# Kernel tuning notes

Hardware: AMD Instinct MI355X
Metric: run time of the kernel (lower is better)

Reference implementation:

```python
import jax, jax.numpy as jnp
import numpy as np

B = 8
INPUT_SIZE = 32        # fc output dim == res row length
RESAMPLING = 500       # chunk width; 500->250->125->62->31 under 4 stride-2 pools
CHUNKS = 15            # == channel_size; seq length T = CHUNKS * RESAMPLING
T = CHUNKS * RESAMPLING
EPS = 1e-5
FC_IN = 32 * 6 * 31    # 5952 = flattened (C,H,W) embedding output


def _conv2d(x, w, b, pad):
    y = jax.lax.conv_general_dilated(x, w, (1, 1), pad,
                                     dimension_numbers=('NCHW', 'OIHW', 'NCHW'))
    return y + b[None, :, None, None]


def _bn(x, g, beta, m, v):
    # eval-mode BatchNorm2d with running stats
    scale = g / jnp.sqrt(v + EPS)
    return (x - m[None, :, None, None]) * scale[None, :, None, None] + beta[None, :, None, None]


def _maxpool22(x):
    return jax.lax.reduce_window(x, -jnp.inf, jax.lax.max, (1, 1, 2, 2), (1, 1, 2, 2), 'VALID')


def _forward(x, w1, b1, g1, beta1, m1, v1, w2, b2, g2, beta2, m2, v2,
             w3, b3, g3, beta3, m3, v3, w4, b4, g4, beta4, m4, v4,
             wfc, bfc, wc3, bc3, wout, bout):
    bsz = x.shape[0]
    # Vectorize the original per-sample / per-chunk Python loops:
    # split each [100, T] sample into CHUNKS windows of width RESAMPLING.
    h = x[:, 0].reshape(bsz, 100, CHUNKS, RESAMPLING)
    h = h.transpose(0, 2, 1, 3).reshape(bsz * CHUNKS, 1, 100, RESAMPLING)
    for w, b, g, bt, m, v in ((w1, b1, g1, beta1, m1, v1),
                              (w2, b2, g2, beta2, m2, v2),
                              (w3, b3, g3, beta3, m3, v3),
                              (w4, b4, g4, beta4, m4, v4)):
        h = _maxpool22(jax.nn.relu(_bn(_conv2d(h, w, b, [(2, 2), (2, 2)]), g, bt, m, v)))
    feats = h.reshape(bsz * CHUNKS, FC_IN)          # torch flattens in (C,H,W) order
    res = feats @ wfc.T + bfc                       # [B*15, 32]
    r = res.reshape(bsz, CHUNKS, INPUT_SIZE)[..., None]  # [B, 15, 32, 1] (NCHW)

    pad_c = lambda t: jnp.pad(t, ((0, 0), (0, 0), (1, 1), (0, 0)))   # ZeroPad2d((0,0,1,1))
    conv3 = lambda t: _conv2d(t, wc3, bc3, [(0, 0), (0, 0)])          # (3,1) conv
    r = conv3(jax.nn.relu(pad_c(r)))
    r = conv3(jax.nn.relu(pad_c(r)))
    while r.shape[2] > 2:  # static shapes: H 32->16->8->4->2
        p = jnp.pad(r, ((0, 0), (0, 0), (0, 1), (0, 0)))              # ZeroPad2d((0,0,0,1))
        px = jax.lax.reduce_window(p, -jnp.inf, jax.lax.max, (1, 1, 3, 1), (1, 1, 2, 2), 'VALID')
        t = conv3(jax.nn.relu(pad_c(px)))
        t = conv3(jax.nn.relu(pad_c(t)))
        r = t + px
    return r.reshape(bsz, 2 * CHUNKS) @ wout.T + bout  # [B, 2]


def setup_inputs() -> dict:
    key = jax.random.key(0)
    ks = jax.random.split(key, 16)

    def rn(k, shape, s):
        return jax.random.normal(k, shape, jnp.float32) * s

    inp = {"x": jax.random.normal(ks[0], (B, 1, 100, T), jnp.float32)}
    chans = [(1, 16), (16, 32), (32, 64), (64, 32)]
    for i, (ci, co) in enumerate(chans, 1):
        inp[f"w{i}"] = rn(ks[i], (co, ci, 5, 5), (2.0 / (ci * 25)) ** 0.5)
        inp[f"b{i}"] = jnp.zeros((co,), jnp.float32)
        inp[f"g{i}"] = jnp.ones((co,), jnp.float32)
        inp[f"beta{i}"] = jnp.zeros((co,), jnp.float32)
        inp[f"m{i}"] = jnp.zeros((co,), jnp.float32)
        inp[f"v{i}"] = jnp.ones((co,), jnp.float32)
    inp["wfc"] = rn(ks[5], (INPUT_SIZE, FC_IN), FC_IN ** -0.5)
    inp["bfc"] = jnp.zeros((INPUT_SIZE,), jnp.float32)
    inp["wc3"] = rn(ks[6], (CHUNKS, CHUNKS, 3, 1), (CHUNKS * 3) ** -0.5)
    inp["bc3"] = jnp.zeros((CHUNKS,), jnp.float32)
    inp["wout"] = rn(ks[7], (2, 2 * CHUNKS), (2 * CHUNKS) ** -0.5)
    inp["bout"] = jnp.zeros((2,), jnp.float32)
    return inp


def reference(x, w1, b1, g1, beta1, m1, v1, w2, b2, g2, beta2, m2, v2,
              w3, b3, g3, beta3, m3, v3, w4, b4, g4, beta4, m4, v4,
              wfc, bfc, wc3, bc3, wout, bout):
    return _forward(x, w1, b1, g1, beta1, m1, v1, w2, b2, g2, beta2, m2, v2,
                    w3, b3, g3, beta3, m3, v3, w4, b4, g4, beta4, m4, v4,
                    wfc, bfc, wc3, bc3, wout, bout)
```

## Files before the change

### kernel.cpp

```cpp
#include <hip/hip_runtime.h>
#include <hip/hip_bf16.h>

#define EPS 1e-5f

typedef short bf16x8 __attribute__((ext_vector_type(8)));
typedef float f32x4  __attribute__((ext_vector_type(4)));

__device__ __forceinline__ unsigned short f2bf(float f) {
    __hip_bfloat16 h = __float2bfloat16(f);
    return *(unsigned short*)&h;
}
__device__ __forceinline__ float bf2f(unsigned short u) {
    __hip_bfloat16 h = *(__hip_bfloat16*)&u;
    return __bfloat162float(h);
}

__device__ __forceinline__ void packA(const float* __restrict__ w,
                                      unsigned short* __restrict__ Apk,
                                      int i, int CI, int COTALL)
{
    const int j = i & 7, lane = (i >> 3) & 63, pc = i >> 9;
    const int p = pc / COTALL, cot = pc % COTALL;
    const int kidx = p * 32 + (lane >> 4) * 8 + j;
    const int tap = kidx / CI, ci = kidx % CI;
    const int co = cot * 16 + (lane & 15);
    Apk[i] = f2bf((tap < 25) ? w[((size_t)co * CI + ci) * 25 + tap] : 0.f);
}

__global__ void prep_all(
    const float* w1, const float* w2, const float* w3, const float* w4,
    const float* wfc,
    const float* g1, const float* be1, const float* m1, const float* v1, const float* b1,
    const float* g2, const float* be2, const float* m2, const float* v2, const float* b2,
    const float* g3, const float* be3, const float* m3, const float* v3, const float* b3,
    const float* g4, const float* be4, const float* m4, const float* v4, const float* b4,
    float* scsh, unsigned short* A1, unsigned short* A2, unsigned short* A3,
    unsigned short* A4, unsigned short* wfcT)
{
    constexpr int S0 = 144, S1 = S0 + 512, S2 = S1 + 13312;
    constexpr int S3 = S2 + 51200, S4 = S3 + 51200, S5 = S4 + 190464;
    const int idx = blockIdx.x * 256 + threadIdx.x;
    if (idx < S0) {
        const int t = idx;
        if (t < 32) {
            const float sc = g2[t] / sqrtf(v2[t] + EPS);
            scsh[t] = sc; scsh[32 + t] = (b2[t] - m2[t]) * sc + be2[t];
        } else if (t < 96) {
            const int c = t - 32;
            const float sc = g3[c] / sqrtf(v3[c] + EPS);
            scsh[64 + c] = sc; scsh[128 + c] = (b3[c] - m3[c]) * sc + be3[c];
        } else if (t < 128) {
            const int c = t - 96;
            const float sc = g4[c] / sqrtf(v4[c] + EPS);
            scsh[192 + c] = sc; scsh[224 + c] = (b4[c] - m4[c]) * sc + be4[c];
        } else {
            const int c = t - 128;
            const float sc = g1[c] / sqrtf(v1[c] + EPS);
            scsh[256 + c] = sc; scsh[272 + c] = (b1[c] - m1[c]) * sc + be1[c];
        }
    } else if (idx < S1) {
        const int i = idx - S0;
        const int j = i & 7, lane = i >> 3;
        const int k = ((lane >> 4) & 3) * 8 + j;
        A1[i] = f2bf((k < 25) ? w1[(lane & 15) * 25 + k] : 0.f);
    } else if (idx < S2) {
        packA(w2, A2, idx - S1, 16, 2);
    } else if (idx < S3) {
        packA(w3, A3, idx - S2, 32, 4);
    } else if (idx < S4) {
        packA(w4, A4, idx - S3, 64, 2);
    } else if (idx < S5) {
        const int i = idx - S4;
        const int o = i / 5952, j = i % 5952;
        const int c = j & 31, yx = j >> 5;
        wfcT[i] = f2bf(wfc[(size_t)o * 5952 + c * 186 + yx]);
    }
}

__global__ __launch_bounds__(256) void conv1_mfma(
    const float* __restrict__ x,
    const unsigned short* __restrict__ Apk1,
    const float* __restrict__ sc, const float* __restrict__ sh,
    unsigned short* __restrict__ out)
{
    constexpr int RSTR = 70;
    __shared__ unsigned short tile[12 * RSTR];
    const int n = blockIdx.z;
    const int y0 = blockIdx.y * 8, x0 = blockIdx.x * 64;
    const int b = n / 15, c = n % 15;
    const float* xb = x + (size_t)b * 100 * 7500 + (size_t)c * 500;
    const int tid = threadIdx.x;

    for (int i = tid; i < 12 * 68; i += 256) {
        const int yy = i / 68, xx = i % 68;
        const int gy = y0 - 2 + yy, gx = x0 - 2 + xx;
        float v = 0.f;
        if (gy >= 0 && gy < 100 && gx >= 0 && gx < 500) v = xb[gy * 7500 + gx];
        tile[yy * RSTR + xx] = f2bf(v);
    }

    const int lane = tid & 63, wav = tid >> 6;
    const int g = lane >> 4, c15 = lane & 15;
    const bf16x8 a = *(const bf16x8*)(Apk1 + lane * 8);

    int off[8];
    #pragma unroll
    for (int j = 0; j < 8; ++j) {
        int tap = g * 8 + j;
        if (tap > 24) tap = 24;
        off[j] = (tap / 5) * RSTR + (tap % 5);
    }
    __syncthreads();

    f32x4 acc[2][4] = {};
    #pragma unroll
    for (int r = 0; r < 2; ++r)
        #pragma unroll
        for (int cg = 0; cg < 4; ++cg) {
            const int base = (2 * wav + r) * RSTR + cg * 16 + c15;
            bf16x8 bfrag;
            #pragma unroll
            for (int j = 0; j < 8; ++j)
                ((unsigned short*)&bfrag)[j] = (short)tile[base + off[j]];
            acc[r][cg] = __builtin_amdgcn_mfma_f32_16x16x32_bf16(a, bfrag, acc[r][cg], 0, 0, 0);
        }

    const int py = blockIdx.y * 4 + wav;
    const float4 scv = *(const float4*)(sc + g * 4);
    const float4 shv = *(const float4*)(sh + g * 4);
    #pragma unroll
    for (int cg = 0; cg < 4; ++cg) {
        const int px = (x0 >> 1) + cg * 8 + (c15 >> 1);
        ushort4 st;
        #pragma unroll
        for (int reg = 0; reg < 4; ++reg) {
            const float scr = (&scv.x)[reg], shr = (&shv.x)[reg];
            const float v0 = fmaxf(acc[0][cg][reg] * scr + shr, 0.f);
            const float v1 = fmaxf(acc[1][cg][reg] * scr + shr, 0.f);
            float mx = fmaxf(v0, v1);
            mx = fmaxf(mx, __shfl_xor(mx, 1));
            (&st.x)[reg] = f2bf(mx);
        }
        if ((lane & 1) == 0 && py < 50 && px < 250)
            *(ushort4*)(out + (((size_t)n * 50 + py) * 250 + px) * 16 + g * 4) = st;
    }
}

template <int CI, int CO, int H, int W, int PH, int PW, int NP, int NCT>
__global__ __launch_bounds__(256) void mfma_conv(
    const unsigned short* __restrict__ in,
    const unsigned short* __restrict__ Apk,
    const float* __restrict__ sc, const float* __restrict__ sh,
    unsigned short* __restrict__ outp)
{
    constexpr int TH = 8, TW = 32, ROWS = TH + 4, COLS = TW + 4;
    constexpr int CPC = CI / 8;
    constexpr int PLANESZ = ROWS * COLS * 16;
    constexpr int PPAD = (CPC == 2) ? 64 : (CPC == 4 ? 32 : 16);
    constexpr int PSTR = PLANESZ + PPAD;
    constexpr int COTALL = CO / 16;
    constexpr int COB = CO / (16 * NCT);
    __shared__ char smem[CPC * PSTR];

    const int n = blockIdx.z / COB, cob = blockIdx.z % COB;
    const int ytile = blockIdx.y * TH, xtile = blockIdx.x * TW;
    const int tid = threadIdx.x;

    for (int i = tid; i < ROWS * COLS * CPC; i += 256) {
        const int cell = i / CPC, ch = i % CPC;
        const int yy = cell / COLS, xx = cell % COLS;
        const int gy = ytile - 2 + yy, gx = xtile - 2 + xx;
        uint4 val = make_uint4(0, 0, 0, 0);
        if (gy >= 0 && gy < H && gx >= 0 && gx < W)
            val = *(const uint4*)(in + ((((size_t)n * H + gy) * W + gx) * CI + ch * 8));
        *(uint4*)(smem + ch * PSTR + cell * 16) = val;
    }
    __syncthreads();

    const int lane = tid & 63, wav = tid >> 6;
    const int g = lane >> 4, c15 = lane & 15;
    const bool hi = (lane >= 32);
    const int plane = (CI == 16) ? (g & 1) : g;
    const char* bbase = smem + plane * PSTR + ((wav * 2) * COLS + c15) * 16;

    f32x4 acc[2][NCT][2] = {};

    #pragma unroll
    for (int p = 0; p < NP; ++p) {
        int Dv = 0;
        if (CI == 16) {
            int t0 = p * 2;     if (t0 > 24) t0 = 24;
            int t1 = p * 2 + 1; if (t1 > 24) t1 = 24;
            const int D0 = ((t0 / 5) * COLS + t0 % 5) * 16;
            const int D1 = ((t1 / 5) * COLS + t1 % 5) * 16;
            Dv = hi ? D1 : D0;
        }
        const int tap = (CI == 32) ? p : ((CI == 64) ? (p >> 1) : 0);
        const int pimm = (CI == 64) ? (p & 1) * 4 * PSTR : 0;

        bf16x8 a[NCT], b[2][2];
        #pragma unroll
        for (int ct = 0; ct < NCT; ++ct)
            a[ct] = *(const bf16x8*)(Apk +
                ((size_t)(p * COTALL + cob * NCT + ct) * 64 + lane) * 8);
        #pragma unroll
        for (int r = 0; r < 2; ++r)
            #pragma unroll
            for (int cg = 0; cg < 2; ++cg) {
                const int imm = (CI == 16)
                    ? (r * COLS + cg * 16) * 16
                    : (((r + tap / 5) * COLS + cg * 16 + tap % 5) * 16 + pimm);
                b[r][cg] = *(const bf16x8*)(bbase + Dv + imm);
            }
        #pragma unroll
        for (int r = 0; r < 2; ++r)
            #pragma unroll
            for (int ct = 0; ct < NCT; ++ct)
                #pragma unroll
                for (int cg = 0; cg < 2; ++cg)
                    acc[r][ct][cg] = __builtin_amdgcn_mfma_f32_16x16x32_bf16(
                        a[ct], b[r][cg], acc[r][ct][cg], 0, 0, 0);
    }

    const int py = blockIdx.y * 4 + wav;
    #pragma unroll
    for (int ct = 0; ct < NCT; ++ct) {
        const int coW = (cob * NCT + ct) * 16;
        const float4 scv = *(const float4*)(sc + coW + g * 4);
        const float4 shv = *(const float4*)(sh + coW + g * 4);
        #pragma unroll
        for (int cg = 0; cg < 2; ++cg) {
            const int px = (xtile >> 1) + cg * 8 + (c15 >> 1);
            ushort4 st;
            #pragma unroll
            for (int reg = 0; reg < 4; ++reg) {
                const float scr = (&scv.x)[reg], shr = (&shv.x)[reg];
                const float v0 = fmaxf(acc[0][ct][cg][reg] * scr + shr, 0.f);
                const float v1 = fmaxf(acc[1][ct][cg][reg] * scr + shr, 0.f);
                float mx = fmaxf(v0, v1);
                mx = fmaxf(mx, __shfl_xor(mx, 1));
                (&st.x)[reg] = f2bf(mx);
            }
            if ((lane & 1) == 0 && py < PH && px < PW)
                *(ushort4*)(outp + (((size_t)n * PH + py) * PW + px) * CO + coW + g * 4) = st;
        }
    }
}

__global__ __launch_bounds__(256) void fc_kernel(
    const unsigned short* __restrict__ feats, const unsigned short* __restrict__ wfcT,
    const float* __restrict__ bfc, float* __restrict__ res)
{
    const int n = blockIdx.x;
    const int lane = threadIdx.x & 63;
    const int wave = threadIdx.x >> 6;
    const unsigned short* f = feats + (size_t)n * 5952;
    #pragma unroll
    for (int o8 = 0; o8 < 8; ++o8) {
        const int o = wave * 8 + o8;
        const unsigned short* wr = wfcT + (size_t)o * 5952;
        float s = 0.f;
        #pragma unroll
        for (int i = 0; i < 12; ++i) {
            const int j8 = (i * 64 + lane) * 8;
            if (j8 < 5952) {
                const bf16x8 fv = *(const bf16x8*)(f + j8);
                const bf16x8 wv = *(const bf16x8*)(wr + j8);
                #pragma unroll
                for (int q = 0; q < 8; ++q)
                    s += bf2f(((const unsigned short*)&fv)[q]) *
                         bf2f(((const unsigned short*)&wv)[q]);
            }
        }
        #pragma unroll
        for (int off = 32; off > 0; off >>= 1) s += __shfl_down(s, off, 64);
        if (lane == 0) res[n * 32 + o] = s + bfc[o];
    }
}

__global__ __launch_bounds__(512) void dpcnn_kernel(
    const float* __restrict__ res,
    const float* __restrict__ wc3, const float* __restrict__ bc3,
    const float* __restrict__ wout, const float* __restrict__ bout,
    float* __restrict__ out)
{
    __shared__ float rr[8][15][32];
    __shared__ float ar[8][15][34];
    __shared__ float tr[8][15][34];
    __shared__ float px[8][15][16];
    __shared__ float wk[15][45];
    __shared__ float bk[15];

    const int tid = threadIdx.x;
    for (int i = tid; i < 15 * 45; i += 512) ((float*)wk)[i] = wc3[i];
    if (tid < 15) bk[tid] = bc3[tid];
    for (int i = tid; i < 8 * 15 * 32; i += 512) {
        const int h = i & 31, c = (i >> 5) % 15, b = i / 480;
        const float val = res[i];
        rr[b][c][h] = val;
        ar[b][c][h + 1] = fmaxf(val, 0.f);
    }
    for (int i = tid; i < 8 * 15; i += 512) {
        const int c = i % 15, b = i / 15;
        ar[b][c][0] = 0.f; ar[b][c][33] = 0.f;
        tr[b][c][0] = 0.f; tr[b][c][33] = 0.f;
    }
    __syncthreads();

    #define CONV45(SRC, BCH, CCH, HH)                                          \
        float s0 = bk[CCH], s1 = 0.f, s2 = 0.f;                                \
        {                                                                      \
            const float* srow = &SRC[BCH][0][HH];                              \
            const float* wrow = &wk[CCH][0];                                   \
            _Pragma("unroll")                                                  \
            for (int ci = 0; ci < 15; ++ci) {                                  \
                s0 += wrow[ci * 3 + 0] * srow[ci * 34 + 0];                    \
                s1 += wrow[ci * 3 + 1] * srow[ci * 34 + 1];                    \
                s2 += wrow[ci * 3 + 2] * srow[ci * 34 + 2];                    \
            }                                                                  \
        }                                                                      \
        const float val = s0 + s1 + s2;

    {
        for (int i = tid; i < 8 * 15 * 32; i += 512) {
            const int h = i & 31, cc = (i >> 5) % 15, b = i / 480;
            CONV45(ar, b, cc, h)
            tr[b][cc][h + 1] = fmaxf(val, 0.f);
        }
        __syncthreads();
        for (int i = tid; i < 8 * 15 * 32; i += 512) {
            const int h = i & 31, cc = (i >> 5) % 15, b = i / 480;
            CONV45(tr, b, cc, h)
            rr[b][cc][h] = val;
            ar[b][cc][h + 1] = fmaxf(val, 0.f);
        }
        __syncthreads();
    }

    for (int H = 32; H > 2; H >>= 1) {
        const int Hh = H >> 1;
        const int NE = 8 * 15 * Hh;
        for (int i = tid; i < NE; i += 512) {
            const int h = i % Hh, cc = (i / Hh) % 15, b = i / (15 * Hh);
            const float m0 = rr[b][cc][2 * h], m1 = rr[b][cc][2 * h + 1];
            const float m2 = (2 * h + 2 < H) ? rr[b][cc][2 * h + 2] : 0.f;
            const float pv = fmaxf(fmaxf(m0, m1), m2);
            px[b][cc][h] = pv;
            ar[b][cc][h + 1] = fmaxf(pv, 0.f);
            if (h == 0) ar[b][cc][0] = 0.f;
            if (h == Hh - 1) ar[b][cc][Hh + 1] = 0.f;
        }
        __syncthreads();
        for (int i = tid; i < NE; i += 512) {
            const int h = i % Hh, cc = (i / Hh) % 15, b = i / (15 * Hh);
            CONV45(ar, b, cc, h)
            tr[b][cc][h + 1] = fmaxf(val, 0.f);
            if (h == 0) tr[b][cc][0] = 0.f;
            if (h == Hh - 1) tr[b][cc][Hh + 1] = 0.f;
        }
        __syncthreads();
        for (int i = tid; i < NE; i += 512) {
            const int h = i % Hh, cc = (i / Hh) % 15, b = i / (15 * Hh);
            CONV45(tr, b, cc, h)
            const float rv = val + px[b][cc][h];
            rr[b][cc][h] = rv;
            ar[b][cc][h + 1] = fmaxf(rv, 0.f);
        }
        __syncthreads();
    }
    #undef CONV45

    if (tid < 16) {
        const int b = tid >> 1, o = tid & 1;
        float s = bout[o];
        for (int c = 0; c < 15; ++c)
            #pragma unroll
            for (int h = 0; h < 2; ++h)
                s += wout[o * 30 + c * 2 + h] * rr[b][c][h];
        out[b * 2 + o] = s;
    }
}

extern "C" void kernel_launch(void* const* d_in, const int* in_sizes, int n_in,
                              void* d_out, int out_size, void* d_ws, size_t ws_size,
                              hipStream_t stream)
{
    const float* x = (const float*)d_in[0];
    const float* w1 = (const float*)d_in[1];  const float* b1 = (const float*)d_in[2];
    const float* g1 = (const float*)d_in[3];  const float* be1 = (const float*)d_in[4];
    const float* m1 = (const float*)d_in[5];  const float* v1 = (const float*)d_in[6];
    const float* w2 = (const float*)d_in[7];  const float* b2 = (const float*)d_in[8];
    const float* g2 = (const float*)d_in[9];  const float* be2 = (const float*)d_in[10];
    const float* m2 = (const float*)d_in[11]; const float* v2 = (const float*)d_in[12];
    const float* w3 = (const float*)d_in[13]; const float* b3 = (const float*)d_in[14];
    const float* g3 = (const float*)d_in[15]; const float* be3 = (const float*)d_in[16];
    const float* m3 = (const float*)d_in[17]; const float* v3 = (const float*)d_in[18];
    const float* w4 = (const float*)d_in[19]; const float* b4 = (const float*)d_in[20];
    const float* g4 = (const float*)d_in[21]; const float* be4 = (const float*)d_in[22];
    const float* m4 = (const float*)d_in[23]; const float* v4 = (const float*)d_in[24];
    const float* wfc = (const float*)d_in[25]; const float* bfc = (const float*)d_in[26];
    const float* wc3 = (const float*)d_in[27]; const float* bc3 = (const float*)d_in[28];
    const float* wout = (const float*)d_in[29]; const float* bout = (const float*)d_in[30];
    float* out = (float*)d_out;

    (void)in_sizes; (void)n_in; (void)out_size; (void)ws_size;

    float* wsf = (float*)d_ws;
    float* res   = wsf;
    float* scsh  = wsf + 3840;
    float* sc2 = scsh, *sh2 = scsh + 32;
    float* sc3 = scsh + 64, *sh3 = scsh + 128;
    float* sc4 = scsh + 192, *sh4 = scsh + 224;
    float* sc1 = scsh + 256, *sh1 = scsh + 272;
    unsigned short* A1  = (unsigned short*)(wsf + 4160);
    unsigned short* A2  = (unsigned short*)(wsf + 4416);
    unsigned short* A3  = (unsigned short*)(wsf + 11072);
    unsigned short* A4  = (unsigned short*)(wsf + 36672);
    unsigned short* c1o = (unsigned short*)(wsf + 62272);
    unsigned short* c2o = (unsigned short*)(wsf + 12062272);
    unsigned short* c3o = (unsigned short*)(wsf + 18062272);
    unsigned short* c4o = (unsigned short*)(wsf + 20919232);
    unsigned short* wfcT = (unsigned short*)(wsf + 21276352);

    prep_all<<<1199, 256, 0, stream>>>(
        w1, w2, w3, w4, wfc,
        g1, be1, m1, v1, b1, g2, be2, m2, v2, b2,
        g3, be3, m3, v3, b3, g4, be4, m4, v4, b4,
        scsh, A1, A2, A3, A4, wfcT);

    conv1_mfma<<<dim3(8, 13, 120), 256, 0, stream>>>(x, A1, sc1, sh1, c1o);
    mfma_conv<16, 32, 50, 250, 25, 125, 13, 2><<<dim3(8, 7, 120), 256, 0, stream>>>(
        c1o, A2, sc2, sh2, c2o);
    mfma_conv<32, 64, 25, 125, 12, 62, 25, 4><<<dim3(4, 3, 120), 256, 0, stream>>>(
        c2o, A3, sc3, sh3, c3o);
    mfma_conv<64, 32, 12, 62, 6, 31, 50, 2><<<dim3(2, 2, 120), 256, 0, stream>>>(
        c3o, A4, sc4, sh4, c4o);
    fc_kernel<<<dim3(120), 256, 0, stream>>>(c4o, wfcT, bfc, res);
    dpcnn_kernel<<<dim3(1), 512, 0, stream>>>(res, wc3, bc3, wout, bout, out);
}
```

Measured before the change: 322.8 us.

## Fuse conv4 with FC layer per sample and widen conv2 tiles

Conv4 and the fully connected layer now run in one 512-thread kernel per sample. It stages the conv3 output in 16-channel slices through shared memory, keeps the pooled features in LDS and computes the FC dot products directly from them. This removes one launch and the global round trip of the conv4 output. The A4 weight packing is changed to match the new per-16-channel tap-pair order. The conv template gains a tile-width parameter and conv2 uses 64-wide tiles, halving its grid width. Only 120 blocks run the fused kernel, with 6 of 8 waves doing MFMA work, so parallelism may drop.

New measurement: 306.7 us. 5.0% less time.

```diff
diff --git a/kernel.cpp b/kernel.cpp
--- a/kernel.cpp
+++ b/kernel.cpp
@@ -38,7 +38,7 @@
     unsigned short* A4, unsigned short* wfcT)
 {
     constexpr int S0 = 144, S1 = S0 + 512, S2 = S1 + 13312;
-    constexpr int S3 = S2 + 51200, S4 = S3 + 51200, S5 = S4 + 190464;
+    constexpr int S3 = S2 + 51200, S4 = S3 + 53248, S5 = S4 + 190464;
     const int idx = blockIdx.x * 256 + threadIdx.x;
     if (idx < S0) {
         const int t = idx;
@@ -68,7 +68,15 @@
     } else if (idx < S3) {
         packA(w3, A3, idx - S2, 32, 4);
     } else if (idx < S4) {
-        packA(w4, A4, idx - S3, 64, 2);
+        const int i = idx - S3;
+        const int j = i & 7, lane = (i >> 3) & 63, pc = i >> 9;
+        const int p = pc >> 1, ct = pc & 1;
+        const int g = lane >> 4;
+        const int tp = p % 13, qt = p / 13;
+        const int tap = tp * 2 + (g >> 1);
+        const int ci = qt * 16 + (g & 1) * 8 + j;
+        const int co = ct * 16 + (lane & 15);
+        A4[i] = f2bf((tap < 25) ? w4[((size_t)co * 64 + ci) * 25 + tap] : 0.f);
     } else if (idx < S5) {
         const int i = idx - S4;
         const int o = i / 5952, j = i % 5952;
@@ -146,14 +154,14 @@
     }
 }
 
-template <int CI, int CO, int H, int W, int PH, int PW, int NP, int NCT>
+template <int CI, int CO, int H, int W, int PH, int PW, int NP, int NCT, int TWP>
 __global__ __launch_bounds__(256) void mfma_conv(
     const unsigned short* __restrict__ in,
     const unsigned short* __restrict__ Apk,
     const float* __restrict__ sc, const float* __restrict__ sh,
     unsigned short* __restrict__ outp)
 {
-    constexpr int TH = 8, TW = 32, ROWS = TH + 4, COLS = TW + 4;
+    constexpr int TH = 8, COLS = TWP + 4, ROWS = TH + 4, NCG = TWP / 16;
     constexpr int CPC = CI / 8;
     constexpr int PLANESZ = ROWS * COLS * 16;
     constexpr int PPAD = (CPC == 2) ? 64 : (CPC == 4 ? 32 : 16);
@@ -163,7 +171,7 @@
     __shared__ char smem[CPC * PSTR];
 
     const int n = blockIdx.z / COB, cob = blockIdx.z % COB;
-    const int ytile = blockIdx.y * TH, xtile = blockIdx.x * TW;
+    const int ytile = blockIdx.y * TH, xtile = blockIdx.x * TWP;
     const int tid = threadIdx.x;
 
     for (int i = tid; i < ROWS * COLS * CPC; i += 256) {
@@ -183,7 +191,7 @@
     const int plane = (CI == 16) ? (g & 1) : g;
     const char* bbase = smem + plane * PSTR + ((wav * 2) * COLS + c15) * 16;
 
-    f32x4 acc[2][NCT][2] = {};
+    f32x4 acc[2][NCT][NCG] = {};
 
     #pragma unroll
     for (int p = 0; p < NP; ++p) {
@@ -198,7 +206,7 @@
         const int tap = (CI == 32) ? p : ((CI == 64) ? (p >> 1) : 0);
         const int pimm = (CI == 64) ? (p & 1) * 4 * PSTR : 0;
 
-        bf16x8 a[NCT], b[2][2];
+        bf16x8 a[NCT], b[2][NCG];
         #pragma unroll
         for (int ct = 0; ct < NCT; ++ct)
             a[ct] = *(const bf16x8*)(Apk +
@@ -206,7 +214,7 @@
         #pragma unroll
         for (int r = 0; r < 2; ++r)
             #pragma unroll
-            for (int cg = 0; cg < 2; ++cg) {
+            for (int cg = 0; cg < NCG; ++cg) {
                 const int imm = (CI == 16)
                     ? (r * COLS + cg * 16) * 16
                     : (((r + tap / 5) * COLS + cg * 16 + tap % 5) * 16 + pimm);
@@ -217,7 +225,7 @@
             #pragma unroll
             for (int ct = 0; ct < NCT; ++ct)
                 #pragma unroll
-                for (int cg = 0; cg < 2; ++cg)
+                for (int cg = 0; cg < NCG; ++cg)
                     acc[r][ct][cg] = __builtin_amdgcn_mfma_f32_16x16x32_bf16(
                         a[ct], b[r][cg], acc[r][ct][cg], 0, 0, 0);
     }
@@ -229,7 +237,7 @@
         const float4 scv = *(const float4*)(sc + coW + g * 4);
         const float4 shv = *(const float4*)(sh + coW + g * 4);
         #pragma unroll
-        for (int cg = 0; cg < 2; ++cg) {
+        for (int cg = 0; cg < NCG; ++cg) {
             const int px = (xtile >> 1) + cg * 8 + (c15 >> 1);
             ushort4 st;
             #pragma unroll
@@ -247,24 +255,108 @@
     }
 }
 
-__global__ __launch_bounds__(256) void fc_kernel(
-    const unsigned short* __restrict__ feats, const unsigned short* __restrict__ wfcT,
+__global__ __launch_bounds__(512) void conv4fc_kernel(
+    const unsigned short* __restrict__ in,
+    const unsigned short* __restrict__ Apk,
+    const float* __restrict__ sc, const float* __restrict__ sh,
+    const unsigned short* __restrict__ wfcT,
     const float* __restrict__ bfc, float* __restrict__ res)
 {
+    constexpr int COLS = 66, ROWS = 16;
+    constexpr int PLANESZ = ROWS * COLS * 16;
+    constexpr int PSTR = PLANESZ + 32;
+    __shared__ char smem[2 * PSTR + 6 * 31 * 32 * 2];
+    unsigned short* feats = (unsigned short*)(smem + 2 * PSTR);
+
     const int n = blockIdx.x;
-    const int lane = threadIdx.x & 63;
-    const int wave = threadIdx.x >> 6;
-    const unsigned short* f = feats + (size_t)n * 5952;
+    const int tid = threadIdx.x;
+    const int lane = tid & 63, wav = tid >> 6;
+    const int g = lane >> 4, c15 = lane & 15;
+    const bool hi = (lane >= 32);
+
+    const char* bbase = smem + (g & 1) * PSTR + ((wav * 2) * COLS + c15) * 16;
+    f32x4 acc[2][2][4] = {};
+
+    for (int qt = 0; qt < 4; ++qt) {
+        __syncthreads();
+        for (int i = tid; i < ROWS * COLS * 2; i += 512) {
+            const int pl = i & 1, cell = i >> 1;
+            const int row = cell / COLS, col = cell - row * COLS;
+            const int gy = row - 2, gx = col - 2;
+            uint4 val = make_uint4(0, 0, 0, 0);
+            if (gy >= 0 && gy < 12 && gx >= 0 && gx < 62)
+                val = *(const uint4*)(in +
+                    ((((size_t)n * 12 + gy) * 62 + gx) * 64 + qt * 16 + pl * 8));
+            *(uint4*)(smem + pl * PSTR + cell * 16) = val;
+        }
+        __syncthreads();
+        if (wav < 6) {
+            #pragma unroll
+            for (int tp = 0; tp < 13; ++tp) {
+                const int p = qt * 13 + tp;
+                int t0 = tp * 2;     if (t0 > 24) t0 = 24;
+                int t1 = tp * 2 + 1; if (t1 > 24) t1 = 24;
+                const int D0 = ((t0 / 5) * COLS + t0 % 5) * 16;
+                const int D1 = ((t1 / 5) * COLS + t1 % 5) * 16;
+                const int Dv = hi ? D1 : D0;
+                bf16x8 a[2], b[2][4];
+                #pragma unroll
+                for (int ct = 0; ct < 2; ++ct)
+                    a[ct] = *(const bf16x8*)(Apk + ((size_t)(p * 2 + ct) * 64 + lane) * 8);
+                #pragma unroll
+                for (int r = 0; r < 2; ++r)
+                    #pragma unroll
+                    for (int cg = 0; cg < 4; ++cg)
+                        b[r][cg] = *(const bf16x8*)(bbase + Dv + (r * COLS + cg * 16) * 16);
+                #pragma unroll
+                for (int r = 0; r < 2; ++r)
+                    #pragma unroll
+                    for (int ct = 0; ct < 2; ++ct)
+                        #pragma unroll
+                        for (int cg = 0; cg < 4; ++cg)
+                            acc[r][ct][cg] = __builtin_amdgcn_mfma_f32_16x16x32_bf16(
+                                a[ct], b[r][cg], acc[r][ct][cg], 0, 0, 0);
+            }
+        }
+    }
+
+    if (wav < 6) {
+        const int py = wav;
+        #pragma unroll
+        for (int ct = 0; ct < 2; ++ct) {
+            const int coW = ct * 16;
+            const float4 scv = *(const float4*)(sc + coW + g * 4);
+            const float4 shv = *(const float4*)(sh + coW + g * 4);
+            #pragma unroll
+            for (int cg = 0; cg < 4; ++cg) {
+                const int px = cg * 8 + (c15 >> 1);
+                ushort4 st;
+                #pragma unroll
+                for (int reg = 0; reg < 4; ++reg) {
+                    const float scr = (&scv.x)[reg], shr = (&shv.x)[reg];
+                    const float v0 = fmaxf(acc[0][ct][cg][reg] * scr + shr, 0.f);
+                    const float v1 = fmaxf(acc[1][ct][cg][reg] * scr + shr, 0.f);
+                    float mx = fmaxf(v0, v1);
+                    mx = fmaxf(mx, __shfl_xor(mx, 1));
+                    (&st.x)[reg] = f2bf(mx);
+                }
+                if ((lane & 1) == 0 && px < 31)
+                    *(ushort4*)(feats + (py * 31 + px) * 32 + coW + g * 4) = st;
+            }
+        }
+    }
+    __syncthreads();
+
     #pragma unroll
-    for (int o8 = 0; o8 < 8; ++o8) {
-        const int o = wave * 8 + o8;
+    for (int oi = 0; oi < 4; ++oi) {
+        const int o = wav * 4 + oi;
         const unsigned short* wr = wfcT + (size_t)o * 5952;
         float s = 0.f;
         #pragma unroll
-        for (int i = 0; i < 12; ++i) {
-            const int j8 = (i * 64 + lane) * 8;
+        for (int ii = 0; ii < 12; ++ii) {
+            const int j8 = (ii * 64 + lane) * 8;
             if (j8 < 5952) {
-                const bf16x8 fv = *(const bf16x8*)(f + j8);
+                const bf16x8 fv = *(const bf16x8*)(feats + j8);
                 const bf16x8 wv = *(const bf16x8*)(wr + j8);
                 #pragma unroll
                 for (int q = 0; q < 8; ++q)
@@ -416,25 +508,23 @@
     unsigned short* A2  = (unsigned short*)(wsf + 4416);
     unsigned short* A3  = (unsigned short*)(wsf + 11072);
     unsigned short* A4  = (unsigned short*)(wsf + 36672);
-    unsigned short* c1o = (unsigned short*)(wsf + 62272);
-    unsigned short* c2o = (unsigned short*)(wsf + 12062272);
-    unsigned short* c3o = (unsigned short*)(wsf + 18062272);
-    unsigned short* c4o = (unsigned short*)(wsf + 20919232);
-    unsigned short* wfcT = (unsigned short*)(wsf + 21276352);
-
-    prep_all<<<1199, 256, 0, stream>>>(
+    unsigned short* c1o = (unsigned short*)(wsf + 63360);
+    unsigned short* c2o = (unsigned short*)(wsf + 12063360);
+    unsigned short* c3o = (unsigned short*)(wsf + 18063360);
+    unsigned short* wfcT = (unsigned short*)(wsf + 20920320);
+
+    prep_all<<<1207, 256, 0, stream>>>(
         w1, w2, w3, w4, wfc,
         g1, be1, m1, v1, b1, g2, be2, m2, v2, b2,
         g3, be3, m3, v3, b3, g4, be4, m4, v4, b4,
         scsh, A1, A2, A3, A4, wfcT);
 
     conv1_mfma<<<dim3(8, 13, 120), 256, 0, stream>>>(x, A1, sc1, sh1, c1o);
-    mfma_conv<16, 32, 50, 250, 25, 125, 13, 2><<<dim3(8, 7, 120), 256, 0, stream>>>(
+    mfma_conv<16, 32, 50, 250, 25, 125, 13, 2, 64><<<dim3(4, 7, 120), 256, 0, stream>>>(
         c1o, A2, sc2, sh2, c2o);
-    mfma_conv<32, 64, 25, 125, 12, 62, 25, 4><<<dim3(4, 3, 120), 256, 0, stream>>>(
+    mfma_conv<32, 64, 25, 125, 12, 62, 25, 4, 32><<<dim3(4, 3, 120), 256, 0, stream>>>(
         c2o, A3, sc3, sh3, c3o);
-    mfma_conv<64, 32, 12, 62, 6, 31, 50, 2><<<dim3(2, 2, 120), 256, 0, stream>>>(
-        c3o, A4, sc4, sh4, c4o);
-    fc_kernel<<<dim3(120), 256, 0, stream>>>(c4o, wfcT, bfc, res);
+    conv4fc_kernel<<<dim3(120), 512, 0, stream>>>(
+        c3o, A4, sc4, sh4, wfcT, bfc, res);
     dpcnn_kernel<<<dim3(1), 512, 0, stream>>>(res, wc3, bc3, wout, bout, out);
 }
```
